# Kernel tuning notes

Hardware: AMD Instinct MI355X
Metric: run time of the kernel (lower is better)

The kernel has to match this reference:

```python
import jax, jax.numpy as jnp
import numpy as np

EPS_RMS = 1.1920929e-07  # torch F.rms_norm default eps = finfo(float32).eps
N_EMBD = 64
N_QKV = 256


def _silu(t):
    return t * jax.nn.sigmoid(t)


def _rms_norm(t):
    return t * jax.lax.rsqrt(jnp.mean(t * t, axis=-1, keepdims=True) + EPS_RMS)


def _w_norm(w, n):
    target_std = n ** (-0.5)
    return w * (target_std / (jnp.std(w, ddof=1) + 1e-08))


def setup_inputs() -> dict:
    key = jax.random.key(0)
    ks = jax.random.split(key, 7)
    B, T = 8, 8192
    x = jax.random.normal(ks[0], (B, T, N_EMBD), dtype=jnp.float32)
    y = jax.random.normal(ks[1], (B, T, N_QKV), dtype=jnp.float32)
    # CastedLinear init: uniform(-s, s), s = sqrt(3)/sqrt(in_features)
    def lin(k, out_f, in_f):
        s = (3.0 ** 0.5) * in_f ** (-0.5)
        return jax.random.uniform(k, (out_f, in_f), jnp.float32, -s, s)
    w_qkv = lin(ks[2], 3 * N_QKV, N_EMBD)          # [768, 64]
    w_swiglu = lin(ks[3], 2 * N_EMBD, N_QKV)       # [128, 256]
    w_out = lin(ks[4], N_EMBD, N_EMBD)             # [64, 64]
    out_w = lin(ks[5], N_EMBD, N_EMBD)             # self.out weight [64, 64]
    tao = lin(ks[6], 3, 1)                          # [3, 1]
    return {"x": x, "y": y, "w_qkv": w_qkv, "w_swiglu": w_swiglu,
            "w_out": w_out, "out_w": out_w, "tao": tao}


def reference(x, y, w_qkv, w_swiglu, w_out, out_w, tao):
    B = x.shape[0]
    # SwiGLU branch: F.linear(y, w_swiglu) -> [B,T,2*n_embd], chunk
    uv = jnp.einsum('btq,eq->bte', y, w_swiglu)
    u, v = jnp.split(uv, 2, axis=-1)                 # each [B,T,64]
    y_out = x + jnp.einsum('btd,ed->bte', u * _silu(v), w_out)

    # gates
    g = jnp.clip(jnp.abs(tao), 1e-08, 1.0)           # [3,1]
    alpha, beta, gamma = g[0], g[1], g[2]

    # Hebbian outer-product memory: mean_b(u^T v) * n_embd^-0.5, rms-normed
    ao = jnp.einsum('btd,bte->de', u, v) / B * (N_EMBD ** (-0.5))  # [64,64]
    ao = _rms_norm(ao)

    # update w_qkv
    n1 = _silu(w_qkv @ ao)                            # [768,64]
    w_qkv_new = _w_norm(w_qkv + n1 @ out_w.T, N_EMBD) * alpha

    # update w_swiglu: view(64, 512).T @ ao
    n2 = _silu(w_swiglu.reshape(N_EMBD, 2 * N_QKV).T @ ao)  # [512,64]
    n2 = n2 @ out_w.T                                  # [512,64]
    w_swiglu_new = w_swiglu + n2.T.reshape(2 * N_EMBD, N_QKV)
    w_swiglu_new = _w_norm(w_swiglu_new, N_QKV) * beta

    # update w_out
    n3 = _silu(w_out @ ao)                             # [64,64]
    w_out_new = _w_norm(w_out + n3 @ out_w.T, N_QKV) * gamma

    return (y_out, w_qkv_new, w_swiglu_new, w_out_new)
```

## Files before the change

kernel.cpp:

```cpp
#include <hip/hip_runtime.h>
#include <cstdint>

typedef short short8 __attribute__((ext_vector_type(8)));
typedef short short4_t __attribute__((ext_vector_type(4)));
typedef float floatx4 __attribute__((ext_vector_type(4)));

#define MFMA_BF16 __builtin_amdgcn_mfma_f32_16x16x32_bf16

__device__ __forceinline__ short f2bf(float f) {
  union { float f; unsigned u; } a; a.f = f;
  unsigned r = a.u + 0x7FFFu + ((a.u >> 16) & 1u);
  return (short)(r >> 16);
}
__device__ __forceinline__ float bf2f(short s) {
  union { unsigned u; float f; } a;
  a.u = ((unsigned)(unsigned short)s) << 16;
  return a.f;
}
__device__ __forceinline__ float silu_f(float v) {
  return v / (1.0f + __expf(-v));
}

#define QDIM 256
#define DEMB 64
#define TILE_T 32
#define ITERS 2
#define NBLK1 1024
#define YSTR 264
#define TSTR 40
#define HSTR 72

#define OFF_QKV 4194304
#define OFF_SW  4243456
#define OFF_WO  4276224

#define AO_COPIES 16
#define WS_SUMS   65536
#define WS_AOT    65544

__global__ __launch_bounds__(256, 2) void k1_main(
    const float* __restrict__ x, const float* __restrict__ y,
    const float* __restrict__ w_sw, const float* __restrict__ w_out,
    float* __restrict__ y_out, float* __restrict__ ao_copies)
{
  __shared__ __align__(16) short Ylds[TILE_T * YSTR];
  __shared__ __align__(16) short UVT[128 * TSTR];
  __shared__ __align__(16) short Hlds[TILE_T * HSTR];

  const int tid  = threadIdx.x;
  const int lane = tid & 63;
  const int wave = tid >> 6;
  const int l15  = lane & 15;
  const int quad = lane >> 4;
  const floatx4 fzero = {0.f, 0.f, 0.f, 0.f};
  const int tok0 = blockIdx.x * (TILE_T * ITERS);

  short8 b1[2][8];
#pragma unroll
  for (int nt = 0; nt < 2; ++nt) {
    const float* wr = w_sw + (size_t)(wave * 32 + nt * 16 + l15) * QDIM;
#pragma unroll
    for (int kt = 0; kt < 8; ++kt) {
      const float* p = wr + kt * 32 + quad * 8;
      short8 f;
#pragma unroll
      for (int j = 0; j < 8; ++j) f[j] = f2bf(p[j]);
      b1[nt][kt] = f;
    }
  }
  short8 b2[2];
  {
    const float* wr = w_out + (size_t)(wave * 16 + l15) * DEMB;
#pragma unroll
    for (int kt = 0; kt < 2; ++kt) {
      const float* p = wr + kt * 32 + quad * 8;
      short8 f;
#pragma unroll
      for (int j = 0; j < 8; ++j) f[j] = f2bf(p[j]);
      b2[kt] = f;
    }
  }

  floatx4 ao_acc[4];
#pragma unroll
  for (int i = 0; i < 4; ++i) ao_acc[i] = fzero;

  for (int it = 0; it < ITERS; ++it) {
    const int tbase = tok0 + it * TILE_T;

    {
      const float4* src = (const float4*)(y + (size_t)tbase * QDIM);
#pragma unroll
      for (int rep = 0; rep < 8; ++rep) {
        int i = tid + rep * 256;
        float4 f = src[i];
        int tok = i >> 6;
        int col = (i & 63) * 4;
        short4_t p4 = { f2bf(f.x), f2bf(f.y), f2bf(f.z), f2bf(f.w) };
        *(short4_t*)&Ylds[tok * YSTR + col] = p4;
      }
    }
    __syncthreads();

    floatx4 acc[2][2];
#pragma unroll
    for (int a = 0; a < 2; ++a)
#pragma unroll
      for (int b = 0; b < 2; ++b) acc[a][b] = fzero;
#pragma unroll
    for (int kt = 0; kt < 8; ++kt) {
      short8 a0 = *(const short8*)&Ylds[(l15)      * YSTR + kt * 32 + quad * 8];
      short8 a1 = *(const short8*)&Ylds[(16 + l15) * YSTR + kt * 32 + quad * 8];
      acc[0][0] = MFMA_BF16(a0, b1[0][kt], acc[0][0], 0, 0, 0);
      acc[0][1] = MFMA_BF16(a0, b1[1][kt], acc[0][1], 0, 0, 0);
      acc[1][0] = MFMA_BF16(a1, b1[0][kt], acc[1][0], 0, 0, 0);
      acc[1][1] = MFMA_BF16(a1, b1[1][kt], acc[1][1], 0, 0, 0);
    }
#pragma unroll
    for (int mt = 0; mt < 2; ++mt)
#pragma unroll
      for (int nt = 0; nt < 2; ++nt) {
        short4_t p4;
#pragma unroll
        for (int r = 0; r < 4; ++r) p4[r] = f2bf(acc[mt][nt][r]);
        int c  = wave * 32 + nt * 16 + l15;
        int t0 = mt * 16 + quad * 4;
        *(short4_t*)&UVT[c * TSTR + t0] = p4;
      }
    __syncthreads();

    {
      int d  = tid & 63;
      int t0 = (tid >> 6) * 8;
      short8 u8 = *(const short8*)&UVT[d * TSTR + t0];
      short8 v8 = *(const short8*)&UVT[(64 + d) * TSTR + t0];
#pragma unroll
      for (int j = 0; j < 8; ++j) {
        float h = bf2f(u8[j]) * silu_f(bf2f(v8[j]));
        Hlds[(t0 + j) * HSTR + d] = f2bf(h);
      }
    }
    {
      short8 a3 = *(const short8*)&UVT[(wave * 16 + l15) * TSTR + quad * 8];
#pragma unroll
      for (int et = 0; et < 4; ++et) {
        short8 b3 = *(const short8*)&UVT[(64 + et * 16 + l15) * TSTR + quad * 8];
        ao_acc[et] = MFMA_BF16(a3, b3, ao_acc[et], 0, 0, 0);
      }
    }
    __syncthreads();

#pragma unroll
    for (int mt = 0; mt < 2; ++mt) {
      floatx4 acc2 = fzero;
#pragma unroll
      for (int kt = 0; kt < 2; ++kt) {
        short8 a2 = *(const short8*)&Hlds[(mt * 16 + l15) * HSTR + kt * 32 + quad * 8];
        acc2 = MFMA_BF16(a2, b2[kt], acc2, 0, 0, 0);
      }
      int e = wave * 16 + l15;
#pragma unroll
      for (int r = 0; r < 4; ++r) {
        size_t idx = (size_t)(tbase + mt * 16 + quad * 4 + r) * DEMB + e;
        y_out[idx] = x[idx] + acc2[r];
      }
    }
  }

  float* dst = ao_copies + (blockIdx.x & (AO_COPIES - 1)) * 4096;
#pragma unroll
  for (int et = 0; et < 4; ++et)
#pragma unroll
    for (int r = 0; r < 4; ++r) {
      int d = wave * 16 + quad * 4 + r;
      int e = et * 16 + l15;
      atomicAdd(&dst[d * 64 + e], ao_acc[et][r]);
    }
}

__global__ __launch_bounds__(256) void k2_finalize(
    const float* __restrict__ ao_copies, unsigned short* __restrict__ aoT)
{
  __shared__ float aoFT[64 * 65];
  __shared__ float ssPart[256];
  __shared__ float scRow[64];
  const int tid = threadIdx.x;

#pragma unroll
  for (int k = 0; k < 16; ++k) {
    int idx = k * 256 + tid;
    float v = 0.f;
#pragma unroll
    for (int c = 0; c < AO_COPIES; ++c) v += ao_copies[c * 4096 + idx];
    v *= (1.0f / 64.0f);
    int d = idx >> 6, e = idx & 63;
    aoFT[e * 65 + d] = v;
  }
  __syncthreads();
  {
    int d = tid >> 2, q = tid & 3;
    float ssp = 0.f;
#pragma unroll
    for (int e2 = 0; e2 < 16; ++e2) {
      float v = aoFT[(q * 16 + e2) * 65 + d];
      ssp += v * v;
    }
    ssPart[tid] = ssp;
  }
  __syncthreads();
  if (tid < 64) {
    float ss = ssPart[tid * 4] + ssPart[tid * 4 + 1] +
               ssPart[tid * 4 + 2] + ssPart[tid * 4 + 3];
    scRow[tid] = rsqrtf(ss * (1.0f / 64.0f) + 1.1920929e-07f);
  }
  __syncthreads();
#pragma unroll
  for (int k = 0; k < 16; ++k) {
    int j = k * 256 + tid;
    int e = j >> 6, d = j & 63;
    aoT[j] = (unsigned short)f2bf(aoFT[e * 65 + d] * scRow[d]);
  }
}

__global__ __launch_bounds__(64) void k3_updates(
    const float* __restrict__ w_qkv, const float* __restrict__ w_sw,
    const float* __restrict__ w_out, const float* __restrict__ out_w,
    const unsigned short* __restrict__ aoT, float* __restrict__ out,
    float* __restrict__ sums)
{
  __shared__ __align__(16) short Nlds[16 * 72];
  const int lane = threadIdx.x;
  const int l15  = lane & 15;
  const int quad = lane >> 4;
  const int rid  = blockIdx.x;
  const floatx4 fzero = {0.f, 0.f, 0.f, 0.f};
  const short8* aoTv = (const short8*)aoT;

  short8 bf[2][4];
#pragma unroll
  for (int kt = 0; kt < 2; ++kt)
#pragma unroll
    for (int nt = 0; nt < 4; ++nt)
      bf[kt][nt] = aoTv[(nt * 16 + l15) * 8 + kt * 4 + quad];

  short8 af[2];
  if (rid < 48) {
    const float* wr = w_qkv + (size_t)(rid * 16 + l15) * 64;
#pragma unroll
    for (int kt = 0; kt < 2; ++kt) {
      const float* p = wr + kt * 32 + quad * 8;
      short8 f;
#pragma unroll
      for (int j = 0; j < 8; ++j) f[j] = f2bf(p[j]);
      af[kt] = f;
    }
  } else if (rid < 80) {
    int p0 = (rid - 48) * 16;
#pragma unroll
    for (int kt = 0; kt < 2; ++kt) {
      short8 f;
#pragma unroll
      for (int j = 0; j < 8; ++j) {
        int a = kt * 32 + quad * 8 + j;
        f[j] = f2bf(w_sw[a * 512 + p0 + l15]);
      }
      af[kt] = f;
    }
  } else {
    const float* wr = w_out + (size_t)((rid - 80) * 16 + l15) * 64;
#pragma unroll
    for (int kt = 0; kt < 2; ++kt) {
      const float* p = wr + kt * 32 + quad * 8;
      short8 f;
#pragma unroll
      for (int j = 0; j < 8; ++j) f[j] = f2bf(p[j]);
      af[kt] = f;
    }
  }

  floatx4 acc[4];
#pragma unroll
  for (int nt = 0; nt < 4; ++nt) acc[nt] = fzero;
#pragma unroll
  for (int kt = 0; kt < 2; ++kt)
#pragma unroll
    for (int nt = 0; nt < 4; ++nt)
      acc[nt] = MFMA_BF16(af[kt], bf[kt][nt], acc[nt], 0, 0, 0);
#pragma unroll
  for (int nt = 0; nt < 4; ++nt)
#pragma unroll
    for (int r = 0; r < 4; ++r)
      Nlds[(quad * 4 + r) * 72 + nt * 16 + l15] = f2bf(silu_f(acc[nt][r]));
  __syncthreads();

  float s1 = 0.f, s2 = 0.f;
  int matrix;

  if (rid < 48 || rid >= 80) {
    matrix = (rid < 48) ? 0 : 2;
    short8 a2[2];
#pragma unroll
    for (int kt = 0; kt < 2; ++kt)
      a2[kt] = *(const short8*)&Nlds[l15 * 72 + kt * 32 + quad * 8];
    short8 b2[2][4];
#pragma unroll
    for (int nt = 0; nt < 4; ++nt) {
      const float* wr = out_w + (size_t)(nt * 16 + l15) * 64;
#pragma unroll
      for (int kt = 0; kt < 2; ++kt) {
        const float* p = wr + kt * 32 + quad * 8;
        short8 f;
#pragma unroll
        for (int j = 0; j < 8; ++j) f[j] = f2bf(p[j]);
        b2[kt][nt] = f;
      }
    }
    floatx4 acc2[4];
#pragma unroll
    for (int nt = 0; nt < 4; ++nt) acc2[nt] = fzero;
#pragma unroll
    for (int kt = 0; kt < 2; ++kt)
#pragma unroll
      for (int nt = 0; nt < 4; ++nt)
        acc2[nt] = MFMA_BF16(a2[kt], b2[kt][nt], acc2[nt], 0, 0, 0);

    const float* Wsrc = (rid < 48) ? w_qkv : w_out;
    int base_row = (rid < 48) ? rid * 16 : (rid - 80) * 16;
    int off      = (rid < 48) ? OFF_QKV : OFF_WO;
#pragma unroll
    for (int nt = 0; nt < 4; ++nt)
#pragma unroll
      for (int r = 0; r < 4; ++r) {
        int row = base_row + quad * 4 + r;
        int col = nt * 16 + l15;
        float val = Wsrc[row * 64 + col] + acc2[nt][r];
        out[off + row * 64 + col] = val;
        s1 += val; s2 += val * val;
      }
  } else {
    matrix = 1;
    int p0 = (rid - 48) * 16;
    short8 b2[2];
#pragma unroll
    for (int kt = 0; kt < 2; ++kt)
      b2[kt] = *(const short8*)&Nlds[l15 * 72 + kt * 32 + quad * 8];
    short8 a2[4][2];
#pragma unroll
    for (int mt = 0; mt < 4; ++mt) {
      const float* wr = out_w + (size_t)(mt * 16 + l15) * 64;
#pragma unroll
      for (int kt = 0; kt < 2; ++kt) {
        const float* p = wr + kt * 32 + quad * 8;
        short8 f;
#pragma unroll
        for (int j = 0; j < 8; ++j) f[j] = f2bf(p[j]);
        a2[mt][kt] = f;
      }
    }
    floatx4 acc2[4];
#pragma unroll
    for (int mt = 0; mt < 4; ++mt) acc2[mt] = fzero;
#pragma unroll
    for (int mt = 0; mt < 4; ++mt)
#pragma unroll
      for (int kt = 0; kt < 2; ++kt)
        acc2[mt] = MFMA_BF16(a2[mt][kt], b2[kt], acc2[mt], 0, 0, 0);
#pragma unroll
    for (int mt = 0; mt < 4; ++mt)
#pragma unroll
      for (int r = 0; r < 4; ++r) {
        int a = mt * 16 + quad * 4 + r;
        int p = p0 + l15;
        int idx = a * 512 + p;
        float val = w_sw[idx] + acc2[mt][r];
        out[OFF_SW + idx] = val;
        s1 += val; s2 += val * val;
      }
  }

#pragma unroll
  for (int off = 32; off > 0; off >>= 1) {
    s1 += __shfl_down(s1, off);
    s2 += __shfl_down(s2, off);
  }
  if (lane == 0) {
    atomicAdd(&sums[matrix * 2],     s1);
    atomicAdd(&sums[matrix * 2 + 1], s2);
  }
}

__global__ __launch_bounds__(256) void k4_scale(
    float* __restrict__ out, const float* __restrict__ sums,
    const float* __restrict__ tao)
{
  int i = blockIdx.x * 256 + threadIdx.x;
  int matrix, idx; float N, tstd;
  if (i < 49152)      { matrix = 0; idx = OFF_QKV + i;           N = 49152.f; tstd = 0.125f;  }
  else if (i < 81920) { matrix = 1; idx = OFF_SW + (i - 49152);  N = 32768.f; tstd = 0.0625f; }
  else                { matrix = 2; idx = OFF_WO + (i - 81920);  N = 4096.f;  tstd = 0.0625f; }
  float sum = sums[matrix * 2], sumsq = sums[matrix * 2 + 1];
  float mean = sum / N;
  float var  = (sumsq - N * mean * mean) / (N - 1.f);
  float sd   = sqrtf(fmaxf(var, 0.f));
  float g    = fminf(fmaxf(fabsf(tao[matrix]), 1e-8f), 1.0f);
  out[idx] *= g * tstd / (sd + 1e-8f);
}

extern "C" void kernel_launch(void* const* d_in, const int* in_sizes, int n_in,
                              void* d_out, int out_size, void* d_ws, size_t ws_size,
                              hipStream_t stream) {
  const float* x     = (const float*)d_in[0];
  const float* y     = (const float*)d_in[1];
  const float* w_qkv = (const float*)d_in[2];
  const float* w_sw  = (const float*)d_in[3];
  const float* w_out = (const float*)d_in[4];
  const float* out_w = (const float*)d_in[5];
  const float* tao   = (const float*)d_in[6];
  float* out = (float*)d_out;
  float* ws  = (float*)d_ws;

  float* ao_copies    = ws;
  float* sums         = ws + WS_SUMS;
  unsigned short* aoT = (unsigned short*)(ws + WS_AOT);

  hipMemsetAsync(d_ws, 0, (WS_SUMS + 8) * sizeof(float), stream);
  k1_main<<<dim3(NBLK1), dim3(256), 0, stream>>>(x, y, w_sw, w_out, out, ao_copies);
  k2_finalize<<<dim3(1), dim3(256), 0, stream>>>(ao_copies, aoT);
  k3_updates<<<dim3(84), dim3(64), 0, stream>>>(w_qkv, w_sw, w_out, out_w,
                                                aoT, out, sums);
  k4_scale<<<dim3(336), dim3(256), 0, stream>>>(out, sums, tao);
}
```

Measured before the change: 155.1 us.

## Pre-pack bf16 weight fragments and double-buffer y tiles in main kernel

Adds a small pre-pass kernel that converts the SwiGLU and output weights into bf16 MFMA fragment layout once, so each main-kernel block loads packed fragments instead of converting fp32 weights itself. The main kernel now handles four tiles per block with half as many blocks, prefetches the next y tile into registers and double-buffers it in LDS, and defers the output projection of the previous tile so it overlaps the next tile's loads. x values are also loaded into registers early. This costs an extra kernel launch, more registers and LDS, and fewer blocks for latency hiding.

New measurement: 142.6 us. 8.1% less time.

```diff
diff --git a/kernel.cpp b/kernel.cpp
--- a/kernel.cpp
+++ b/kernel.cpp
@@ -24,8 +24,8 @@
 #define QDIM 256
 #define DEMB 64
 #define TILE_T 32
-#define ITERS 2
-#define NBLK1 1024
+#define ITERS 4
+#define NBLK1 512
 #define YSTR 264
 #define TSTR 40
 #define HSTR 72
@@ -37,13 +37,42 @@
 #define AO_COPIES 16
 #define WS_SUMS   65536
 #define WS_AOT    65544
+#define WS_W1P    67592
+#define WS_W2P    83976
+
+__global__ __launch_bounds__(256) void k0_pack(
+    const float* __restrict__ w_sw, const float* __restrict__ w_out,
+    short* __restrict__ W1P, short* __restrict__ W2P)
+{
+  int t = blockIdx.x * 256 + threadIdx.x;
+  if (t < 4096) {
+    int lane = t & 63, kt = (t >> 6) & 7, ntw = t >> 9;
+    int row = (ntw >> 1) * 32 + (ntw & 1) * 16 + (lane & 15);
+    int col = kt * 32 + (lane >> 4) * 8;
+    const float* p = w_sw + row * QDIM + col;
+    short8 f;
+#pragma unroll
+    for (int j = 0; j < 8; ++j) f[j] = f2bf(p[j]);
+    ((short8*)W1P)[t] = f;
+  } else {
+    int u = t - 4096;
+    int lane = u & 63, ktw = u >> 6;
+    int row = (ktw >> 1) * 16 + (lane & 15);
+    int col = (ktw & 1) * 32 + (lane >> 4) * 8;
+    const float* p = w_out + row * DEMB + col;
+    short8 f;
+#pragma unroll
+    for (int j = 0; j < 8; ++j) f[j] = f2bf(p[j]);
+    ((short8*)W2P)[u] = f;
+  }
+}
 
 __global__ __launch_bounds__(256, 2) void k1_main(
     const float* __restrict__ x, const float* __restrict__ y,
-    const float* __restrict__ w_sw, const float* __restrict__ w_out,
+    const short* __restrict__ W1P, const short* __restrict__ W2P,
     float* __restrict__ y_out, float* __restrict__ ao_copies)
 {
-  __shared__ __align__(16) short Ylds[TILE_T * YSTR];
+  __shared__ __align__(16) short Ylds[2][TILE_T * YSTR];
   __shared__ __align__(16) short UVT[128 * TSTR];
   __shared__ __align__(16) short Hlds[TILE_T * HSTR];
 
@@ -55,62 +84,76 @@
   const floatx4 fzero = {0.f, 0.f, 0.f, 0.f};
   const int tok0 = blockIdx.x * (TILE_T * ITERS);
 
+  const short8* W1v = (const short8*)W1P;
+  const short8* W2v = (const short8*)W2P;
   short8 b1[2][8];
 #pragma unroll
-  for (int nt = 0; nt < 2; ++nt) {
-    const float* wr = w_sw + (size_t)(wave * 32 + nt * 16 + l15) * QDIM;
+  for (int nt = 0; nt < 2; ++nt)
+#pragma unroll
+    for (int kt = 0; kt < 8; ++kt)
+      b1[nt][kt] = W1v[((wave * 2 + nt) * 8 + kt) * 64 + lane];
+  short8 b2[2];
+#pragma unroll
+  for (int kt = 0; kt < 2; ++kt)
+    b2[kt] = W2v[(wave * 2 + kt) * 64 + lane];
+
+  floatx4 ao_acc[4];
+#pragma unroll
+  for (int i = 0; i < 4; ++i) ao_acc[i] = fzero;
+
+  float4 yreg[8];
+  {
+    const float4* src = (const float4*)(y + (size_t)tok0 * QDIM);
+#pragma unroll
+    for (int rep = 0; rep < 8; ++rep) yreg[rep] = src[tid + rep * 256];
+#pragma unroll
+    for (int rep = 0; rep < 8; ++rep) {
+      int i = tid + rep * 256;
+      int tok = i >> 6;
+      int col = (i & 63) * 4;
+      float4 f = yreg[rep];
+      short4_t p4 = { f2bf(f.x), f2bf(f.y), f2bf(f.z), f2bf(f.w) };
+      *(short4_t*)&Ylds[0][tok * YSTR + col] = p4;
+    }
+  }
+  float xreg[8];
+  __syncthreads();
+
+  for (int it = 0; it < ITERS; ++it) {
+    const int cur = it & 1;
+
+    if (it + 1 < ITERS) {
+      const float4* src = (const float4*)(y + (size_t)(tok0 + (it + 1) * TILE_T) * QDIM);
+#pragma unroll
+      for (int rep = 0; rep < 8; ++rep) yreg[rep] = src[tid + rep * 256];
+    }
+    if (it > 0) {
+      const int tb = tok0 + (it - 1) * TILE_T;
+#pragma unroll
+      for (int mt = 0; mt < 2; ++mt) {
+        floatx4 acc2 = fzero;
+#pragma unroll
+        for (int kt = 0; kt < 2; ++kt) {
+          short8 a2 = *(const short8*)&Hlds[(mt * 16 + l15) * HSTR + kt * 32 + quad * 8];
+          acc2 = MFMA_BF16(a2, b2[kt], acc2, 0, 0, 0);
+        }
+        int e = wave * 16 + l15;
+#pragma unroll
+        for (int r = 0; r < 4; ++r) {
+          size_t idx = (size_t)(tb + mt * 16 + quad * 4 + r) * DEMB + e;
+          y_out[idx] = xreg[mt * 4 + r] + acc2[r];
+        }
+      }
+    }
+    floatx4 acc[2][2];
+#pragma unroll
+    for (int a = 0; a < 2; ++a)
+#pragma unroll
+      for (int b = 0; b < 2; ++b) acc[a][b] = fzero;
 #pragma unroll
     for (int kt = 0; kt < 8; ++kt) {
-      const float* p = wr + kt * 32 + quad * 8;
-      short8 f;
-#pragma unroll
-      for (int j = 0; j < 8; ++j) f[j] = f2bf(p[j]);
-      b1[nt][kt] = f;
-    }
-  }
-  short8 b2[2];
-  {
-    const float* wr = w_out + (size_t)(wave * 16 + l15) * DEMB;
-#pragma unroll
-    for (int kt = 0; kt < 2; ++kt) {
-      const float* p = wr + kt * 32 + quad * 8;
-      short8 f;
-#pragma unroll
-      for (int j = 0; j < 8; ++j) f[j] = f2bf(p[j]);
-      b2[kt] = f;
-    }
-  }
-
-  floatx4 ao_acc[4];
-#pragma unroll
-  for (int i = 0; i < 4; ++i) ao_acc[i] = fzero;
-
-  for (int it = 0; it < ITERS; ++it) {
-    const int tbase = tok0 + it * TILE_T;
-
-    {
-      const float4* src = (const float4*)(y + (size_t)tbase * QDIM);
-#pragma unroll
-      for (int rep = 0; rep < 8; ++rep) {
-        int i = tid + rep * 256;
-        float4 f = src[i];
-        int tok = i >> 6;
-        int col = (i & 63) * 4;
-        short4_t p4 = { f2bf(f.x), f2bf(f.y), f2bf(f.z), f2bf(f.w) };
-        *(short4_t*)&Ylds[tok * YSTR + col] = p4;
-      }
-    }
-    __syncthreads();
-
-    floatx4 acc[2][2];
-#pragma unroll
-    for (int a = 0; a < 2; ++a)
-#pragma unroll
-      for (int b = 0; b < 2; ++b) acc[a][b] = fzero;
-#pragma unroll
-    for (int kt = 0; kt < 8; ++kt) {
-      short8 a0 = *(const short8*)&Ylds[(l15)      * YSTR + kt * 32 + quad * 8];
-      short8 a1 = *(const short8*)&Ylds[(16 + l15) * YSTR + kt * 32 + quad * 8];
+      short8 a0 = *(const short8*)&Ylds[cur][(l15)      * YSTR + kt * 32 + quad * 8];
+      short8 a1 = *(const short8*)&Ylds[cur][(16 + l15) * YSTR + kt * 32 + quad * 8];
       acc[0][0] = MFMA_BF16(a0, b1[0][kt], acc[0][0], 0, 0, 0);
       acc[0][1] = MFMA_BF16(a0, b1[1][kt], acc[0][1], 0, 0, 0);
       acc[1][0] = MFMA_BF16(a1, b1[0][kt], acc[1][0], 0, 0, 0);
@@ -129,6 +172,14 @@
       }
     __syncthreads();
 
+    {
+      const float* xb = x + (size_t)(tok0 + it * TILE_T) * DEMB + wave * 16 + l15;
+#pragma unroll
+      for (int mt = 0; mt < 2; ++mt)
+#pragma unroll
+        for (int r = 0; r < 4; ++r)
+          xreg[mt * 4 + r] = xb[(mt * 16 + quad * 4 + r) * DEMB];
+    }
     {
       int d  = tid & 63;
       int t0 = (tid >> 6) * 8;
@@ -148,8 +199,22 @@
         ao_acc[et] = MFMA_BF16(a3, b3, ao_acc[et], 0, 0, 0);
       }
     }
+    if (it + 1 < ITERS) {
+#pragma unroll
+      for (int rep = 0; rep < 8; ++rep) {
+        int i = tid + rep * 256;
+        int tok = i >> 6;
+        int col = (i & 63) * 4;
+        float4 f = yreg[rep];
+        short4_t p4 = { f2bf(f.x), f2bf(f.y), f2bf(f.z), f2bf(f.w) };
+        *(short4_t*)&Ylds[1 - cur][tok * YSTR + col] = p4;
+      }
+    }
     __syncthreads();
-
+  }
+
+  {
+    const int tb = tok0 + (ITERS - 1) * TILE_T;
 #pragma unroll
     for (int mt = 0; mt < 2; ++mt) {
       floatx4 acc2 = fzero;
@@ -161,8 +226,8 @@
       int e = wave * 16 + l15;
 #pragma unroll
       for (int r = 0; r < 4; ++r) {
-        size_t idx = (size_t)(tbase + mt * 16 + quad * 4 + r) * DEMB + e;
-        y_out[idx] = x[idx] + acc2[r];
+        size_t idx = (size_t)(tb + mt * 16 + quad * 4 + r) * DEMB + e;
+        y_out[idx] = xreg[mt * 4 + r] + acc2[r];
       }
     }
   }
@@ -422,9 +487,12 @@
   float* ao_copies    = ws;
   float* sums         = ws + WS_SUMS;
   unsigned short* aoT = (unsigned short*)(ws + WS_AOT);
+  short* W1P          = (short*)(ws + WS_W1P);
+  short* W2P          = (short*)(ws + WS_W2P);
 
   hipMemsetAsync(d_ws, 0, (WS_SUMS + 8) * sizeof(float), stream);
-  k1_main<<<dim3(NBLK1), dim3(256), 0, stream>>>(x, y, w_sw, w_out, out, ao_copies);
+  k0_pack<<<dim3(18), dim3(256), 0, stream>>>(w_sw, w_out, W1P, W2P);
+  k1_main<<<dim3(NBLK1), dim3(256), 0, stream>>>(x, y, W1P, W2P, out, ao_copies);
   k2_finalize<<<dim3(1), dim3(256), 0, stream>>>(ao_copies, aoT);
   k3_updates<<<dim3(84), dim3(64), 0, stream>>>(w_qkv, w_sw, w_out, out_w,
                                                 aoT, out, sums);
```
